# Performance work log

Hardware: AMD Instinct MI355X
Metric: run time of the kernel (lower is better)

## Reference

```python
import jax, jax.numpy as jnp
import numpy as np

B, N1, N2, F = 128, 100, 2000, 128
NC = N1 + N2
T = 10
L0, L1, L2 = 32, 32, 16


def setup_inputs() -> dict:
    key = jax.random.key(0)
    ks = jax.random.split(key, 16)
    atom_types = jnp.array([1, 6, 7, 8, 9, 11, 12, 15, 16, 17], dtype=jnp.int32)
    # per-type MLP params, stacked over type dim T (matches build():
    # stddev 1/sqrt(layer_size) for hidden layers, 0.01 for output, zero biases)
    inp = {
        "frag1_layer": jax.random.normal(ks[0], (B, N1, F), jnp.float32),
        "frag2_layer": jax.random.normal(ks[1], (B, N2, F), jnp.float32),
        "complex_layer": jax.random.normal(ks[2], (B, NC, F), jnp.float32),
        "frag1_z": jax.random.randint(ks[3], (B, N1), 0, 18, jnp.int32),
        "frag2_z": jax.random.randint(ks[4], (B, N2), 0, 18, jnp.int32),
        "complex_z": jax.random.randint(ks[5], (B, NC), 0, 18, jnp.int32),
        "type_w0": jax.random.normal(ks[6], (T, F, L0), jnp.float32) * (1.0 / np.sqrt(L0)),
        "type_b0": jnp.zeros((T, L0), jnp.float32),
        "type_w1": jax.random.normal(ks[7], (T, L0, L1), jnp.float32) * (1.0 / np.sqrt(L1)),
        "type_b1": jnp.zeros((T, L1), jnp.float32),
        "type_w2": jax.random.normal(ks[8], (T, L1, L2), jnp.float32) * (1.0 / np.sqrt(L2)),
        "type_b2": jnp.zeros((T, L2), jnp.float32),
        "out_w": jax.random.normal(ks[9], (T, L2, 1), jnp.float32) * 0.01,
        "out_b": jnp.zeros((T, 1), jnp.float32),
        "atom_types": atom_types,
    }
    return inp


def reference(frag1_layer, frag2_layer, complex_layer, frag1_z, frag2_z, complex_z,
              type_w0, type_b0, type_w1, type_b1, type_w2, type_b2,
              out_w, out_b, atom_types):
    def per_type_energy(x, z):
        # dense compute for ALL atom types, then mask-route (same math as original)
        h = jax.nn.relu(jnp.einsum('bnf,tfh->tbnh', x, type_w0) + type_b0[:, None, None, :])
        h = jax.nn.relu(jnp.einsum('tbnh,thk->tbnk', h, type_w1) + type_b1[:, None, None, :])
        h = jax.nn.relu(jnp.einsum('tbnk,tkm->tbnm', h, type_w2) + type_b2[:, None, None, :])
        o = jnp.einsum('tbnm,tmo->tbno', h, out_w)[..., 0] + out_b[:, None, None, 0]  # [T,B,N]
        mask = z[None, :, :] == atom_types[:, None, None]  # [T,B,N]
        per_atom = jnp.sum(jnp.where(mask, o, jnp.zeros_like(o)), axis=0)  # [B,N]
        return jnp.sum(per_atom, axis=1)  # [B]

    e1 = per_type_energy(frag1_layer, frag1_z)
    e2 = per_type_energy(frag2_layer, frag2_z)
    ec = per_type_energy(complex_layer, complex_z)
    binding = ec - (e1 + e2)
    return binding[:, None]  # [B,1]
```

## Files before the change

kernel.cpp:

```cpp
#include <hip/hip_runtime.h>

#define B_ 128
#define N1_ 100
#define N2_ 2000
#define NC_ 2100
#define F_ 128
#define NT_ 10
#define L0_ 32
#define L1_ 32
#define L2_ 16

#define NA1 (B_*N1_)
#define NA2 (B_*N2_)
#define NAC (B_*NC_)
#define NATOT (NA1+NA2+NAC)
#define NBUCK (NT_*B_)
#define CAP_B 512
#define NFILL (NATOT/256)

#define WT_STRIDEH 11520

#define WS_CURSORS 0
#define WS_WPACK   8192
#define WS_LISTS   (WS_WPACK + NT_*WT_STRIDEH*2)
#define WS_NEEDED  ((size_t)WS_LISTS + (size_t)NBUCK*CAP_B*4)

typedef short bf16x8 __attribute__((ext_vector_type(8)));
typedef float f32x4 __attribute__((ext_vector_type(4)));

#define MFMA(a,b,c) __builtin_amdgcn_mfma_f32_16x16x32_bf16((a),(b),(c),0,0,0)

__device__ __forceinline__ unsigned short f2bf(float f){
  unsigned u = __float_as_uint(f);
  unsigned r = (u + 0x7FFFu + ((u >> 16) & 1u)) >> 16;
  return (unsigned short)r;
}
__device__ __forceinline__ float bf2f(unsigned short h){
  return __uint_as_float(((unsigned)h) << 16);
}

__device__ __forceinline__ void cvt8u(uint4 a, uint4 b, bf16x8& hi, bf16x8& lo){
  unsigned u[8] = {a.x, a.y, a.z, a.w, b.x, b.y, b.z, b.w};
  union { bf16x8 v; unsigned uu[4]; } H, L;
  #pragma unroll
  for (int i = 0; i < 4; ++i){
    unsigned p = u[2*i], qq = u[2*i+1];
    H.uu[i] = __builtin_amdgcn_perm(qq, p, 0x07060302u);
    unsigned ra = __float_as_uint(__uint_as_float(p)  - __uint_as_float(p  & 0xFFFF0000u));
    unsigned rb = __float_as_uint(__uint_as_float(qq) - __uint_as_float(qq & 0xFFFF0000u));
    L.uu[i] = __builtin_amdgcn_perm(rb, ra, 0x07060302u);
  }
  hi = H.v; lo = L.v;
}

__device__ __forceinline__ unsigned packsplit(float h){
  unsigned uh = __float_as_uint(h);
  unsigned tr = uh & 0xFFFF0000u;
  float res = h - __uint_as_float(tr);
  return tr | (__float_as_uint(res) >> 16);
}

__device__ __forceinline__ void unpack8(uint4 p0, uint4 p1, bf16x8& hi, bf16x8& lo){
  unsigned pp[8] = {p0.x, p0.y, p0.z, p0.w, p1.x, p1.y, p1.z, p1.w};
  union { bf16x8 v; unsigned uu[4]; } H, L;
  #pragma unroll
  for (int i = 0; i < 4; ++i){
    H.uu[i] = __builtin_amdgcn_perm(pp[2*i+1], pp[2*i], 0x07060302u);
    L.uu[i] = __builtin_amdgcn_perm(pp[2*i+1], pp[2*i], 0x05040100u);
  }
  hi = H.v; lo = L.v;
}

__device__ __forceinline__ void decode_atom(int g,
    const int* __restrict__ z1, const int* __restrict__ z2, const int* __restrict__ zc,
    int& tensor, int& row, int& b, int& z){
  if (g < NA1){ tensor = 0; row = g; b = g / N1_; z = z1[g]; }
  else if (g < NA1 + NA2){ int i = g - NA1; tensor = 1; row = i; b = i / N2_; z = z2[i]; }
  else { int i = g - NA1 - NA2; tensor = 2; row = i; b = i / NC_; z = zc[i]; }
}


__global__ __launch_bounds__(256) void k_fillprep(
    const int* __restrict__ z1, const int* __restrict__ z2, const int* __restrict__ zc,
    const int* __restrict__ atypes,
    const float* __restrict__ tw0, const float* __restrict__ tb0,
    const float* __restrict__ tw1, const float* __restrict__ tb1,
    const float* __restrict__ tw2, const float* __restrict__ tb2,
    const float* __restrict__ ow, const float* __restrict__ ob,
    unsigned* __restrict__ cursors, unsigned* __restrict__ lists,
    unsigned short* __restrict__ wpack){
  int tid = threadIdx.x;
  if (blockIdx.x >= NFILL){
    int t = blockIdx.x - NFILL;
    unsigned short* base = wpack + (size_t)t * WT_STRIDEH;
    const float* w0 = tw0 + (size_t)t * (F_ * L0_);
    for (int i = tid; i < 4096; i += 256){
      int ks = i >> 10, rem = i & 1023;
      int nt = rem >> 9, rem2 = rem & 511;
      int lane = rem2 >> 3, e = rem2 & 7;
      float f = w0[(ks * 32 + (lane >> 4) * 8 + e) * L0_ + nt * 16 + (lane & 15)];
      unsigned short hi = f2bf(f);
      unsigned short lo = f2bf(f - bf2f(hi));
      int off = (ks * 2 + nt) * 1024 + lane * 8 + e;
      base[off] = hi;
      base[off + 512] = lo;
    }
    const float* w1 = tw1 + (size_t)t * (L0_ * L1_);
    for (int i = tid; i < 1024; i += 256){
      int nt = i >> 9, rem2 = i & 511;
      int lane = rem2 >> 3, e = rem2 & 7;
      float f = w1[((lane >> 4) * 8 + e) * L1_ + nt * 16 + (lane & 15)];
      unsigned short hi = f2bf(f);
      unsigned short lo = f2bf(f - bf2f(hi));
      int off = 8192 + nt * 1024 + lane * 8 + e;
      base[off] = hi;
      base[off + 512] = lo;
    }
    const float* w2 = tw2 + (size_t)t * (L1_ * L2_);
    for (int i = tid; i < 512; i += 256){
      int lane = i >> 3, e = i & 7;
      float f = w2[((lane >> 4) * 8 + e) * L2_ + (lane & 15)];
      unsigned short hi = f2bf(f);
      unsigned short lo = f2bf(f - bf2f(hi));
      int off = 10240 + lane * 8 + e;
      base[off] = hi;
      base[off + 512] = lo;
    }
    float* prm = (float*)(base + 11264);
    if (tid < 32) prm[tid] = tb0[t * L0_ + tid];
    else if (tid < 64) prm[tid] = tb1[t * L1_ + tid - 32];
    else if (tid < 80) prm[tid] = tb2[t * L2_ + tid - 64];
    else if (tid < 96) prm[tid] = ow[t * L2_ + tid - 80];
    else if (tid == 96) prm[96] = ob[t];
    return;
  }
  __shared__ int lut[32];
  __shared__ unsigned lhist[NBUCK];
  __shared__ unsigned lbase[NBUCK];
  for (int i = tid; i < NBUCK; i += 256) lhist[i] = 0u;
  if (tid < 32) lut[tid] = -1;
  __syncthreads();
  if (tid < NT_) lut[atypes[tid] & 31] = tid;
  __syncthreads();
  int g = blockIdx.x * 256 + tid;
  int bucket = -1; unsigned entv = 0u;
  {
    int tensor, row, b, z;
    decode_atom(g, z1, z2, zc, tensor, row, b, z);
    int t = lut[z & 31];
    if (t >= 0){
      bucket = t * B_ + b;
      entv = (unsigned)row | ((unsigned)tensor << 19);
      atomicAdd(&lhist[bucket], 1u);
    }
  }
  __syncthreads();
  for (int i = tid; i < NBUCK; i += 256){
    unsigned c = lhist[i];
    lbase[i] = c ? atomicAdd(&cursors[i], c) : 0u;
    lhist[i] = 0u;
  }
  __syncthreads();
  if (bucket >= 0){
    unsigned rank = atomicAdd(&lhist[bucket], 1u) + lbase[bucket];
    if (rank < CAP_B) lists[(size_t)bucket * CAP_B + rank] = entv;
  }
}


__global__ __launch_bounds__(64, 2) void k_main(
    const float* __restrict__ f1, const float* __restrict__ f2, const float* __restrict__ fc,
    const unsigned short* __restrict__ wpack,
    const unsigned* __restrict__ cursors, const unsigned* __restrict__ lists,
    float* __restrict__ out){
  int bucket = blockIdx.y;
  int count = (int)cursors[bucket];
  if (count > CAP_B) count = CAP_B;
  int quarter = (count + 3) >> 2;
  int lstart = blockIdx.x * quarter;
  int lend = lstart + quarter; if (lend > count) lend = count;
  int mycount = lend - lstart;
  if (mycount <= 0) return;
  int t = bucket >> 7, b = bucket & 127;
  int lane = threadIdx.x, q = lane >> 4, r16 = lane & 15;

  const unsigned* lst = lists + (size_t)bucket * CAP_B;

  const unsigned short* wp = wpack + (size_t)t * WT_STRIDEH;
  bf16x8 w0h[8], w0l[8];
  #pragma unroll
  for (int j = 0; j < 8; ++j){
    w0h[j] = *(const bf16x8*)(wp + j * 1024 + lane * 8);
    w0l[j] = *(const bf16x8*)(wp + j * 1024 + 512 + lane * 8);
  }
  bf16x8 w1h[2], w1l[2];
  #pragma unroll
  for (int j = 0; j < 2; ++j){
    w1h[j] = *(const bf16x8*)(wp + 8192 + j * 1024 + lane * 8);
    w1l[j] = *(const bf16x8*)(wp + 8192 + j * 1024 + 512 + lane * 8);
  }
  bf16x8 w2h = *(const bf16x8*)(wp + 10240 + lane * 8);
  bf16x8 w2l = *(const bf16x8*)(wp + 10240 + 512 + lane * 8);
  const float* prm = (const float*)(wp + 11264);
  float b00 = prm[r16],      b01 = prm[16 + r16];
  float b10 = prm[32 + r16], b11 = prm[48 + r16];
  float b2v = prm[64 + r16], owv = prm[80 + r16], obv = prm[96];

  __shared__ unsigned H0[16][44];
  __shared__ unsigned H1[16][44];

  int ntiles = (mycount + 15) >> 4;

  uint4 P0, P1, P2, P3, P4, P5, P6, P7;
  uint4 Q0, Q1, Q2, Q3, Q4, Q5, Q6, Q7;
  bf16x8 aH[4], aL[4];
  float vacc = 0.0f, ssum = 0.0f;

#define FETCHE(j_) lst[min(lstart + (j_) * 16 + r16, lend - 1)]
#define SIGNOF(e_, j_) ((((j_) * 16 + r16) < mycount) ? (((((e_) >> 19) & 3u) == 2u) ? 1.0f : -1.0f) : 0.0f)
#define LOADT(Ej, R0,R1,R2,R3,R4,R5,R6,R7) { \
    int row_ = (int)((Ej) & 0x7FFFFu); \
    int tn_  = (int)(((Ej) >> 19) & 3u); \
    const float* xr_ = ((tn_ == 0) ? f1 : (tn_ == 1) ? f2 : fc) + (size_t)row_ * F_ + q * 8; \
    R0 = *(const uint4*)(xr_);       R1 = *(const uint4*)(xr_ + 4); \
    R2 = *(const uint4*)(xr_ + 32);  R3 = *(const uint4*)(xr_ + 36); \
    R4 = *(const uint4*)(xr_ + 64);  R5 = *(const uint4*)(xr_ + 68); \
    R6 = *(const uint4*)(xr_ + 96);  R7 = *(const uint4*)(xr_ + 100); }

#define MLPBODY(SGc) { \
    f32x4 c00 = {b00, b00, b00, b00}; \
    f32x4 c01 = {b01, b01, b01, b01}; \
    _Pragma("unroll") \
    for (int ks = 0; ks < 4; ++ks){ \
      c00 = MFMA(aH[ks], w0h[2*ks],   c00); \
      c00 = MFMA(aL[ks], w0h[2*ks],   c00); \
      c00 = MFMA(aH[ks], w0l[2*ks],   c00); \
      c01 = MFMA(aH[ks], w0h[2*ks+1], c01); \
      c01 = MFMA(aL[ks], w0h[2*ks+1], c01); \
      c01 = MFMA(aH[ks], w0l[2*ks+1], c01); \
    } \
    _Pragma("unroll") \
    for (int reg = 0; reg < 4; ++reg){ \
      H0[4 * q + reg][r16]      = packsplit(fmaxf(c00[reg], 0.0f)); \
      H0[4 * q + reg][16 + r16] = packsplit(fmaxf(c01[reg], 0.0f)); \
    } \
    asm volatile("s_waitcnt lgkmcnt(0)" ::: "memory"); \
    __builtin_amdgcn_sched_barrier(0); \
    bf16x8 a1H, a1L; \
    { const unsigned* pr_ = &H0[r16][8 * q]; \
      unpack8(*(const uint4*)pr_, *(const uint4*)(pr_ + 4), a1H, a1L); } \
    f32x4 c10 = {b10, b10, b10, b10}; \
    f32x4 c11 = {b11, b11, b11, b11}; \
    c10 = MFMA(a1H, w1h[0], c10); \
    c10 = MFMA(a1L, w1h[0], c10); \
    c10 = MFMA(a1H, w1l[0], c10); \
    c11 = MFMA(a1H, w1h[1], c11); \
    c11 = MFMA(a1L, w1h[1], c11); \
    c11 = MFMA(a1H, w1l[1], c11); \
    _Pragma("unroll") \
    for (int reg = 0; reg < 4; ++reg){ \
      H1[4 * q + reg][r16]      = packsplit(fmaxf(c10[reg], 0.0f)); \
      H1[4 * q + reg][16 + r16] = packsplit(fmaxf(c11[reg], 0.0f)); \
    } \
    asm volatile("s_waitcnt lgkmcnt(0)" ::: "memory"); \
    __builtin_amdgcn_sched_barrier(0); \
    bf16x8 a2H, a2L; \
    { const unsigned* pr_ = &H1[r16][8 * q]; \
      unpack8(*(const uint4*)pr_, *(const uint4*)(pr_ + 4), a2H, a2L); } \
    f32x4 c2 = {b2v, b2v, b2v, b2v}; \
    c2 = MFMA(a2H, w2h, c2); \
    c2 = MFMA(a2L, w2h, c2); \
    c2 = MFMA(a2H, w2l, c2); \
    _Pragma("unroll") \
    for (int reg = 0; reg < 4; ++reg){ \
      float ov = fmaxf(c2[reg], 0.0f) * owv; \
      float sgm = __shfl((SGc), 4 * q + reg, 64); \
      vacc = fmaf(ov, sgm, vacc); \
    } \
    ssum += (SGc); }

  float sgP, sgQ;
  {
    unsigned e0 = FETCHE(0);
    LOADT(e0, P0, P1, P2, P3, P4, P5, P6, P7);
    sgP = SIGNOF(e0, 0);
  }
  if (ntiles > 1){
    unsigned e1 = FETCHE(1);
    LOADT(e1, Q0, Q1, Q2, Q3, Q4, Q5, Q6, Q7);
    sgQ = SIGNOF(e1, 1);
  } else sgQ = 0.0f;
  unsigned eN = (ntiles > 2) ? FETCHE(2) : 0u;
  unsigned eM = (ntiles > 3) ? FETCHE(3) : 0u;

  for (int it = 0; it < ntiles; it += 2){
    {
      float sgc = sgP;
      cvt8u(P0, P1, aH[0], aL[0]);
      cvt8u(P2, P3, aH[1], aL[1]);
      cvt8u(P4, P5, aH[2], aL[2]);
      cvt8u(P6, P7, aH[3], aL[3]);
      if (it + 2 < ntiles){
        LOADT(eN, P0, P1, P2, P3, P4, P5, P6, P7);
        sgP = SIGNOF(eN, it + 2);
        if (it + 4 < ntiles) eN = FETCHE(it + 4);
      }
      MLPBODY(sgc)
    }
    if (it + 1 >= ntiles) break;
    {
      float sgc = sgQ;
      cvt8u(Q0, Q1, aH[0], aL[0]);
      cvt8u(Q2, Q3, aH[1], aL[1]);
      cvt8u(Q4, Q5, aH[2], aL[2]);
      cvt8u(Q6, Q7, aH[3], aL[3]);
      if (it + 3 < ntiles){
        LOADT(eM, Q0, Q1, Q2, Q3, Q4, Q5, Q6, Q7);
        sgQ = SIGNOF(eM, it + 3);
        if (it + 5 < ntiles) eM = FETCHE(it + 5);
      }
      MLPBODY(sgc)
    }
  }
#undef FETCHE
#undef SIGNOF
#undef LOADT
#undef MLPBODY

  vacc = fmaf(0.25f * obv, ssum, vacc);
  #pragma unroll
  for (int m = 1; m < 64; m <<= 1) vacc += __shfl_xor(vacc, m, 64);
  if (lane == 0) atomicAdd(&out[b], vacc);
}


__global__ __launch_bounds__(256) void k_naive(
    const float* __restrict__ f1, const float* __restrict__ f2, const float* __restrict__ fc,
    const int* __restrict__ z1, const int* __restrict__ z2, const int* __restrict__ zc,
    const float* __restrict__ tw0, const float* __restrict__ tb0,
    const float* __restrict__ tw1, const float* __restrict__ tb1,
    const float* __restrict__ tw2, const float* __restrict__ tb2,
    const float* __restrict__ ow, const float* __restrict__ ob,
    const int* __restrict__ atypes, float* __restrict__ out){
  __shared__ int lut[32];
  int tid = threadIdx.x;
  if (tid < 32) lut[tid] = -1;
  __syncthreads();
  if (tid < NT_) lut[atypes[tid] & 31] = tid;
  __syncthreads();
  int g = blockIdx.x * 256 + tid;
  if (g >= NATOT) return;
  int tensor, row, b, z;
  decode_atom(g, z1, z2, zc, tensor, row, b, z);
  int t = lut[z & 31];
  if (t < 0) return;
  const float* x = ((tensor == 0) ? f1 : (tensor == 1) ? f2 : fc) + (size_t)row * F_;
  float h0[L0_];
  #pragma unroll
  for (int j = 0; j < L0_; ++j) h0[j] = tb0[t * L0_ + j];
  for (int k = 0; k < F_; ++k){
    float xx = x[k];
    const float* wr = tw0 + t * (F_ * L0_) + k * L0_;
    #pragma unroll
    for (int j = 0; j < L0_; ++j) h0[j] = fmaf(xx, wr[j], h0[j]);
  }
  #pragma unroll
  for (int j = 0; j < L0_; ++j) h0[j] = fmaxf(h0[j], 0.0f);
  float h1[L1_];
  #pragma unroll
  for (int j = 0; j < L1_; ++j) h1[j] = tb1[t * L1_ + j];
  for (int k = 0; k < L0_; ++k){
    float hh = h0[k];
    const float* wr = tw1 + t * (L1_ * L1_) + k * L1_;
    #pragma unroll
    for (int j = 0; j < L1_; ++j) h1[j] = fmaf(hh, wr[j], h1[j]);
  }
  #pragma unroll
  for (int j = 0; j < L1_; ++j) h1[j] = fmaxf(h1[j], 0.0f);
  float h2[L2_];
  #pragma unroll
  for (int m = 0; m < L2_; ++m) h2[m] = tb2[t * L2_ + m];
  for (int k = 0; k < L1_; ++k){
    float hh = h1[k];
    const float* wr = tw2 + t * (L1_ * L2_) + k * L2_;
    #pragma unroll
    for (int m = 0; m < L2_; ++m) h2[m] = fmaf(hh, wr[m], h2[m]);
  }
  float o = ob[t];
  #pragma unroll
  for (int m = 0; m < L2_; ++m) o += fmaxf(h2[m], 0.0f) * ow[t * L2_ + m];
  float sgn = (tensor == 2) ? 1.0f : -1.0f;
  atomicAdd(&out[b], sgn * o);
}

extern "C" void kernel_launch(void* const* d_in, const int* in_sizes, int n_in,
                              void* d_out, int out_size, void* d_ws, size_t ws_size,
                              hipStream_t stream){
  const float* f1  = (const float*)d_in[0];
  const float* f2  = (const float*)d_in[1];
  const float* fc  = (const float*)d_in[2];
  const int*   z1  = (const int*)d_in[3];
  const int*   z2  = (const int*)d_in[4];
  const int*   zc  = (const int*)d_in[5];
  const float* tw0 = (const float*)d_in[6];
  const float* tb0 = (const float*)d_in[7];
  const float* tw1 = (const float*)d_in[8];
  const float* tb1 = (const float*)d_in[9];
  const float* tw2 = (const float*)d_in[10];
  const float* tb2 = (const float*)d_in[11];
  const float* ow  = (const float*)d_in[12];
  const float* ob  = (const float*)d_in[13];
  const int* atypes = (const int*)d_in[14];
  float* out = (float*)d_out;

  if (ws_size < WS_NEEDED){
    hipMemsetAsync(d_out, 0, B_ * sizeof(float), stream);
    k_naive<<<(NATOT + 255) / 256, 256, 0, stream>>>(
        f1, f2, fc, z1, z2, zc, tw0, tb0, tw1, tb1, tw2, tb2, ow, ob, atypes, out);
    return;
  }

  unsigned* cursors = (unsigned*)((char*)d_ws + WS_CURSORS);
  unsigned short* wpack = (unsigned short*)((char*)d_ws + WS_WPACK);
  unsigned* lists   = (unsigned*)((char*)d_ws + WS_LISTS);

  hipMemsetAsync(cursors, 0, NBUCK * sizeof(unsigned), stream);
  hipMemsetAsync(d_out, 0, B_ * sizeof(float), stream);
  k_fillprep<<<NFILL + NT_, 256, 0, stream>>>(z1, z2, zc, atypes,
      tw0, tb0, tw1, tb1, tw2, tb2, ow, ob, cursors, lists, wpack);
  dim3 grid(4, NBUCK);
  k_main<<<grid, 64, 0, stream>>>(f1, f2, fc, wpack, cursors, lists, out);
}
```

Baseline: 60.77 us.

## Merge four single-wave blocks per bucket into one block sharing LDS-staged weights

```diff
diff --git a/kernel.cpp b/kernel.cpp
--- a/kernel.cpp
+++ b/kernel.cpp
@@ -88,7 +88,7 @@
     const float* __restrict__ tw2, const float* __restrict__ tb2,
     const float* __restrict__ ow, const float* __restrict__ ob,
     unsigned* __restrict__ cursors, unsigned* __restrict__ lists,
-    unsigned short* __restrict__ wpack){
+    unsigned short* __restrict__ wpack, float* __restrict__ out){
   int tid = threadIdx.x;
   if (blockIdx.x >= NFILL){
     int t = blockIdx.x - NFILL;
@@ -132,6 +132,7 @@
     else if (tid < 80) prm[tid] = tb2[t * L2_ + tid - 64];
     else if (tid < 96) prm[tid] = ow[t * L2_ + tid - 80];
     else if (tid == 96) prm[96] = ob[t];
+    if (t == 0 && tid >= 128 && tid < 128 + B_) out[tid - 128] = 0.0f;
     return;
   }
   __shared__ int lut[32];
@@ -168,46 +169,30 @@
 }
 
 
-__global__ __launch_bounds__(64, 2) void k_main(
+__global__ __launch_bounds__(256, 3) void k_main(
     const float* __restrict__ f1, const float* __restrict__ f2, const float* __restrict__ fc,
     const unsigned short* __restrict__ wpack,
     const unsigned* __restrict__ cursors, const unsigned* __restrict__ lists,
     float* __restrict__ out){
-  int bucket = blockIdx.y;
+  int bucket = blockIdx.x;
   int count = (int)cursors[bucket];
   if (count > CAP_B) count = CAP_B;
+  if (count <= 0) return;
+  int t = bucket >> 7, b = bucket & 127;
+  int tid = threadIdx.x;
+  int wv = tid >> 6, lane = tid & 63, q = lane >> 4, r16 = lane & 15;
+
   int quarter = (count + 3) >> 2;
-  int lstart = blockIdx.x * quarter;
+  int lstart = wv * quarter;
   int lend = lstart + quarter; if (lend > count) lend = count;
   int mycount = lend - lstart;
-  if (mycount <= 0) return;
-  int t = bucket >> 7, b = bucket & 127;
-  int lane = threadIdx.x, q = lane >> 4, r16 = lane & 15;
 
   const unsigned* lst = lists + (size_t)bucket * CAP_B;
 
-  const unsigned short* wp = wpack + (size_t)t * WT_STRIDEH;
-  bf16x8 w0h[8], w0l[8];
-  #pragma unroll
-  for (int j = 0; j < 8; ++j){
-    w0h[j] = *(const bf16x8*)(wp + j * 1024 + lane * 8);
-    w0l[j] = *(const bf16x8*)(wp + j * 1024 + 512 + lane * 8);
-  }
-  bf16x8 w1h[2], w1l[2];
-  #pragma unroll
-  for (int j = 0; j < 2; ++j){
-    w1h[j] = *(const bf16x8*)(wp + 8192 + j * 1024 + lane * 8);
-    w1l[j] = *(const bf16x8*)(wp + 8192 + j * 1024 + 512 + lane * 8);
-  }
-  bf16x8 w2h = *(const bf16x8*)(wp + 10240 + lane * 8);
-  bf16x8 w2l = *(const bf16x8*)(wp + 10240 + 512 + lane * 8);
-  const float* prm = (const float*)(wp + 11264);
-  float b00 = prm[r16],      b01 = prm[16 + r16];
-  float b10 = prm[32 + r16], b11 = prm[48 + r16];
-  float b2v = prm[64 + r16], owv = prm[80 + r16], obv = prm[96];
-
-  __shared__ unsigned H0[16][44];
-  __shared__ unsigned H1[16][44];
+  __shared__ uint4 WLv[WT_STRIDEH / 8];
+  __shared__ unsigned H0[4][16][44];
+  __shared__ unsigned H1[4][16][44];
+  unsigned short* WL = (unsigned short*)WLv;
 
   int ntiles = (mycount + 15) >> 4;
 
@@ -227,27 +212,69 @@
     R4 = *(const uint4*)(xr_ + 64);  R5 = *(const uint4*)(xr_ + 68); \
     R6 = *(const uint4*)(xr_ + 96);  R7 = *(const uint4*)(xr_ + 100); }
 
+  float sgP = 0.0f, sgQ = 0.0f;
+  unsigned eN = 0u, eM = 0u;
+  if (mycount > 0){
+    unsigned e0 = FETCHE(0);
+    LOADT(e0, P0, P1, P2, P3, P4, P5, P6, P7);
+    sgP = SIGNOF(e0, 0);
+    if (ntiles > 1){
+      unsigned e1 = FETCHE(1);
+      LOADT(e1, Q0, Q1, Q2, Q3, Q4, Q5, Q6, Q7);
+      sgQ = SIGNOF(e1, 1);
+    }
+    if (ntiles > 2) eN = FETCHE(2);
+    if (ntiles > 3) eM = FETCHE(3);
+  }
+
+  {
+    const uint4* wp4 = (const uint4*)(wpack + (size_t)t * WT_STRIDEH);
+    for (int i = tid; i < WT_STRIDEH / 8; i += 256) WLv[i] = wp4[i];
+  }
+  __syncthreads();
+  if (mycount <= 0) return;
+
+  bf16x8 w1h[2], w1l[2];
+  #pragma unroll
+  for (int j = 0; j < 2; ++j){
+    w1h[j] = *(const bf16x8*)(WL + 8192 + j * 1024 + lane * 8);
+    w1l[j] = *(const bf16x8*)(WL + 8192 + j * 1024 + 512 + lane * 8);
+  }
+  bf16x8 w2h = *(const bf16x8*)(WL + 10240 + lane * 8);
+  bf16x8 w2l = *(const bf16x8*)(WL + 10240 + 512 + lane * 8);
+  const float* prm = (const float*)(WL + 11264);
+  float b00 = prm[r16],      b01 = prm[16 + r16];
+  float b10 = prm[32 + r16], b11 = prm[48 + r16];
+  float b2v = prm[64 + r16], owv = prm[80 + r16], obv = prm[96];
+
+  unsigned (*H0w)[44] = H0[wv];
+  unsigned (*H1w)[44] = H1[wv];
+
 #define MLPBODY(SGc) { \
     f32x4 c00 = {b00, b00, b00, b00}; \
     f32x4 c01 = {b01, b01, b01, b01}; \
     _Pragma("unroll") \
     for (int ks = 0; ks < 4; ++ks){ \
-      c00 = MFMA(aH[ks], w0h[2*ks],   c00); \
-      c00 = MFMA(aL[ks], w0h[2*ks],   c00); \
-      c00 = MFMA(aH[ks], w0l[2*ks],   c00); \
-      c01 = MFMA(aH[ks], w0h[2*ks+1], c01); \
-      c01 = MFMA(aL[ks], w0h[2*ks+1], c01); \
-      c01 = MFMA(aH[ks], w0l[2*ks+1], c01); \
+      bf16x8 wha = *(const bf16x8*)(WL + (2*ks) * 1024 + lane * 8); \
+      bf16x8 wla = *(const bf16x8*)(WL + (2*ks) * 1024 + 512 + lane * 8); \
+      bf16x8 whb = *(const bf16x8*)(WL + (2*ks+1) * 1024 + lane * 8); \
+      bf16x8 wlb = *(const bf16x8*)(WL + (2*ks+1) * 1024 + 512 + lane * 8); \
+      c00 = MFMA(aH[ks], wha, c00); \
+      c00 = MFMA(aL[ks], wha, c00); \
+      c00 = MFMA(aH[ks], wla, c00); \
+      c01 = MFMA(aH[ks], whb, c01); \
+      c01 = MFMA(aL[ks], whb, c01); \
+      c01 = MFMA(aH[ks], wlb, c01); \
     } \
     _Pragma("unroll") \
     for (int reg = 0; reg < 4; ++reg){ \
-      H0[4 * q + reg][r16]      = packsplit(fmaxf(c00[reg], 0.0f)); \
-      H0[4 * q + reg][16 + r16] = packsplit(fmaxf(c01[reg], 0.0f)); \
+      H0w[4 * q + reg][r16]      = packsplit(fmaxf(c00[reg], 0.0f)); \
+      H0w[4 * q + reg][16 + r16] = packsplit(fmaxf(c01[reg], 0.0f)); \
     } \
     asm volatile("s_waitcnt lgkmcnt(0)" ::: "memory"); \
     __builtin_amdgcn_sched_barrier(0); \
     bf16x8 a1H, a1L; \
-    { const unsigned* pr_ = &H0[r16][8 * q]; \
+    { const unsigned* pr_ = &H0w[r16][8 * q]; \
       unpack8(*(const uint4*)pr_, *(const uint4*)(pr_ + 4), a1H, a1L); } \
     f32x4 c10 = {b10, b10, b10, b10}; \
     f32x4 c11 = {b11, b11, b11, b11}; \
@@ -259,13 +286,13 @@
     c11 = MFMA(a1H, w1l[1], c11); \
     _Pragma("unroll") \
     for (int reg = 0; reg < 4; ++reg){ \
-      H1[4 * q + reg][r16]      = packsplit(fmaxf(c10[reg], 0.0f)); \
-      H1[4 * q + reg][16 + r16] = packsplit(fmaxf(c11[reg], 0.0f)); \
+      H1w[4 * q + reg][r16]      = packsplit(fmaxf(c10[reg], 0.0f)); \
+      H1w[4 * q + reg][16 + r16] = packsplit(fmaxf(c11[reg], 0.0f)); \
     } \
     asm volatile("s_waitcnt lgkmcnt(0)" ::: "memory"); \
     __builtin_amdgcn_sched_barrier(0); \
     bf16x8 a2H, a2L; \
-    { const unsigned* pr_ = &H1[r16][8 * q]; \
+    { const unsigned* pr_ = &H1w[r16][8 * q]; \
       unpack8(*(const uint4*)pr_, *(const uint4*)(pr_ + 4), a2H, a2L); } \
     f32x4 c2 = {b2v, b2v, b2v, b2v}; \
     c2 = MFMA(a2H, w2h, c2); \
@@ -278,20 +305,6 @@
       vacc = fmaf(ov, sgm, vacc); \
     } \
     ssum += (SGc); }
-
-  float sgP, sgQ;
-  {
-    unsigned e0 = FETCHE(0);
-    LOADT(e0, P0, P1, P2, P3, P4, P5, P6, P7);
-    sgP = SIGNOF(e0, 0);
-  }
-  if (ntiles > 1){
-    unsigned e1 = FETCHE(1);
-    LOADT(e1, Q0, Q1, Q2, Q3, Q4, Q5, Q6, Q7);
-    sgQ = SIGNOF(e1, 1);
-  } else sgQ = 0.0f;
-  unsigned eN = (ntiles > 2) ? FETCHE(2) : 0u;
-  unsigned eM = (ntiles > 3) ? FETCHE(3) : 0u;
 
   for (int it = 0; it < ntiles; it += 2){
     {
@@ -425,9 +438,7 @@
   unsigned* lists   = (unsigned*)((char*)d_ws + WS_LISTS);
 
   hipMemsetAsync(cursors, 0, NBUCK * sizeof(unsigned), stream);
-  hipMemsetAsync(d_out, 0, B_ * sizeof(float), stream);
   k_fillprep<<<NFILL + NT_, 256, 0, stream>>>(z1, z2, zc, atypes,
-      tw0, tb0, tw1, tb1, tw2, tb2, ow, ob, cursors, lists, wpack);
-  dim3 grid(4, NBUCK);
-  k_main<<<grid, 64, 0, stream>>>(f1, f2, fc, wpack, cursors, lists, out);
-}
+      tw0, tb0, tw1, tb1, tw2, tb2, ow, ob, cursors, lists, wpack, out);
+  k_main<<<NBUCK, 256, 0, stream>>>(f1, f2, fc, wpack, cursors, lists, out);
+}
```

After: 81.84 us. 1.35x slower.
